# Performance work log

Measured on AMD Instinct MI355X. Metric: run time of the kernel, lower is better.

The kernel has to match this reference:

```python
import jax, jax.numpy as jnp
import numpy as np

DISCOUNT_FACTOR = 0.99
EPS = 1e-8


def setup_inputs() -> dict:
    key = jax.random.key(0)
    k1, k2, k3 = jax.random.split(key, 3)
    B, S = 8192, 1024
    # raw params initialized exactly like the torch module: atanh(target)
    raw_gamma = jnp.arctanh(jnp.array([DISCOUNT_FACTOR], dtype=jnp.float32))
    # create_init_lambda_sequence(0.5, S): linear ramp with mean == AVERAGE_LAMBDA
    lam_init = jnp.linspace(0.1, 0.9, S).astype(jnp.float32)
    raw_lambd = jnp.arctanh(lam_init)
    values = jax.random.normal(k1, (B, S + 1, 1), dtype=jnp.float32)
    rewards = jax.random.normal(k2, (B, S, 1), dtype=jnp.float32)
    dones = jax.random.randint(k3, (B, S, 1), 0, 2).astype(jnp.int32)
    return {
        "raw_gamma": raw_gamma,
        "raw_lambd": raw_lambd,
        "values": values,
        "rewards": rewards,
        "dones": dones,
        "input_seq_len": 1024,
    }


def reference(raw_gamma, raw_lambd, values, rewards, dones, input_seq_len):
    # gamma / lambd properties: tanh then clamp_min(1e-8)
    gamma = jnp.maximum(jnp.tanh(raw_gamma), EPS)[0]            # scalar
    lambd = jnp.maximum(jnp.tanh(raw_lambd), EPS)               # [max_seq_len]
    lam_seq = lambd[-input_seq_len:]                            # [S]

    # ---- update_sum_reward_weights (runs under no_grad in torch) ----
    # backward recurrence: v[t] = gamma * (1 - lam[t] + lam[t] * v[t+1]),  v[S] = 1
    def w_step(v_next, lam_t):
        v_t = gamma * (1.0 - lam_t + lam_t * v_next)
        return v_t, jnp.maximum(1.0 - v_t, EPS)

    _, w = jax.lax.scan(
        w_step,
        jnp.asarray(1.0, values.dtype),
        jax.lax.stop_gradient(lam_seq),
        reverse=True,
    )  # w: [S]
    srw = w / jnp.maximum(w.mean(), EPS)
    sum_reward_weights = jax.lax.stop_gradient(srw)[None, :, None]  # [1, S, 1]

    # ---- calculate_lambda_returns ----
    # ret[t] = r[t] + gamma*(1-done[t]) * ((1-lam[t])*V[t+1] + lam[t]*ret[t+1])
    d = dones.astype(values.dtype)
    v_next = values[:, 1:, :]                                   # [B, S, 1]
    xs = (
        jnp.swapaxes(rewards, 0, 1),   # [S, B, 1]
        jnp.swapaxes(d, 0, 1),         # [S, B, 1]
        jnp.swapaxes(v_next, 0, 1),    # [S, B, 1]
        lam_seq,                       # [S]
    )

    def r_step(ret_next, x):
        r, dn, vn, lam = x
        ret = r + gamma * (1.0 - dn) * ((1.0 - lam) * vn + lam * ret_next)
        return ret, ret

    _, rets = jax.lax.scan(r_step, values[:, -1, :], xs, reverse=True)  # [S, B, 1]
    lambda_returns = jnp.swapaxes(rets, 0, 1)                           # [B, S, 1]
    return lambda_returns, sum_reward_weights
```

## Files before the change

### kernel.cpp

```cpp
#include <hip/hip_runtime.h>
#include <math.h>

#define EPSF 1e-8f

typedef float fvec4 __attribute__((ext_vector_type(4), aligned(4)));

__device__ __forceinline__ void suffix_scan64(float& A, float& B, int lane) {
#pragma unroll
    for (int d = 1; d < 64; d <<= 1) {
        float Ao = __shfl_down(A, d);
        float Bo = __shfl_down(B, d);
        if (lane + d < 64) {
            A = fmaf(B, Ao, A);
            B = B * Bo;
        }
    }
}

__global__ __launch_bounds__(256)
void prep_kernel(const float* __restrict__ raw_gamma,
                 const float* __restrict__ raw_lambd, int lam_off,
                 float* __restrict__ gl, float* __restrict__ gol,
                 float* __restrict__ srw_out, int S)
{
    __shared__ float s_gl[1024];
    __shared__ float s_gol[1024];
    const float gamma = fmaxf(tanhf(raw_gamma[0]), EPSF);
    for (int t = threadIdx.x; t < S; t += 256) {
        float lam = fmaxf(tanhf(raw_lambd[lam_off + t]), EPSF);
        float g1 = gamma * lam;
        float g0 = gamma - g1;
        gl[t] = g1;  gol[t] = g0;
        s_gl[t] = g1; s_gol[t] = g0;
    }
    __syncthreads();
    if (threadIdx.x >= 64) return;
    const int lane = threadIdx.x;
    const int base = lane << 4;

    float a[16], b[16];
#pragma unroll
    for (int j = 0; j < 16; ++j) { a[j] = s_gol[base + j]; b[j] = s_gl[base + j]; }

    float A = a[15], Bc = b[15];
#pragma unroll
    for (int j = 14; j >= 0; --j) { A = fmaf(b[j], A, a[j]); Bc *= b[j]; }
    suffix_scan64(A, Bc, lane);
    float EA = __shfl_down(A, 1);
    float EB = __shfl_down(Bc, 1);
    if (lane == 63) { EA = 0.0f; EB = 1.0f; }

    float v = fmaf(EB, 1.0f, EA);
    float w[16];
    float sum = 0.0f;
#pragma unroll
    for (int j = 15; j >= 0; --j) {
        v = fmaf(b[j], v, a[j]);
        w[j] = fmaxf(1.0f - v, EPSF);
        sum += w[j];
    }
#pragma unroll
    for (int d = 32; d; d >>= 1) sum += __shfl_xor(sum, d);
    float inv = 1.0f / fmaxf(sum / (float)S, EPSF);
#pragma unroll
    for (int j = 0; j < 16; ++j) srw_out[base + j] = w[j] * inv;
}

__global__ __launch_bounds__(256, 4)
void td_main(const float* __restrict__ gl, const float* __restrict__ gol,
             const float* __restrict__ values,
             const float* __restrict__ rewards,
             const int* __restrict__ dones,
             float* __restrict__ out, int B, int S)
{
    const int lane = threadIdx.x & 63;
    const int b = blockIdx.x * 4 + (threadIdx.x >> 6);
    if (b >= B) return;

    const float* rrow = rewards + (size_t)b * S;
    const int*   drow = dones   + (size_t)b * S;
    const float* vrow = values  + (size_t)b * (S + 1);
    float*       orow = out     + (size_t)b * S;
    const int base = lane << 4;

    float4 r4[4]; int4 dd[4]; fvec4 v4[4]; float4 g1[4]; float4 g0[4];
#pragma unroll
    for (int k = 0; k < 4; ++k) {
        r4[k] = *(const float4*)(rrow + base + 4 * k);
        dd[k] = *(const int4*)(drow + base + 4 * k);
        v4[k] = *(const fvec4*)(vrow + base + 4 * k);
        g1[k] = *(const float4*)(gl + base + 4 * k);
        g0[k] = *(const float4*)(gol + base + 4 * k);
    }
    float vS = vrow[S];
    float vb = __shfl_down(v4[0].x, 1);
    if (lane == 63) vb = vS;

    float a[16], bb[16];
#pragma unroll
    for (int k = 0; k < 4; ++k) {
        float vn0 = v4[k].y, vn1 = v4[k].z, vn2 = v4[k].w;
        float vn3 = (k < 3) ? v4[k + 1].x : vb;
        float vn[4] = {vn0, vn1, vn2, vn3};
        float rr[4] = {r4[k].x, r4[k].y, r4[k].z, r4[k].w};
        int   di[4] = {dd[k].x, dd[k].y, dd[k].z, dd[k].w};
        float G1[4] = {g1[k].x, g1[k].y, g1[k].z, g1[k].w};
        float G0[4] = {g0[k].x, g0[k].y, g0[k].z, g0[k].w};
#pragma unroll
        for (int j = 0; j < 4; ++j) {
            float nd = 1.0f - (float)di[j];
            bb[4 * k + j] = G1[j] * nd;
            a[4 * k + j]  = fmaf(G0[j] * vn[j], nd, rr[j]);
        }
    }

    float A = a[15], Bc = bb[15];
#pragma unroll
    for (int j = 14; j >= 0; --j) { A = fmaf(bb[j], A, a[j]); Bc *= bb[j]; }

    suffix_scan64(A, Bc, lane);
    float EA = __shfl_down(A, 1);
    float EB = __shfl_down(Bc, 1);
    if (lane == 63) { EA = 0.0f; EB = 1.0f; }
    float x = fmaf(EB, vS, EA);

    float o[16];
#pragma unroll
    for (int j = 15; j >= 0; --j) {
        x = fmaf(bb[j], x, a[j]);
        o[j] = x;
    }
#pragma unroll
    for (int k = 0; k < 4; ++k)
        *(float4*)(orow + base + 4 * k) =
            make_float4(o[4 * k], o[4 * k + 1], o[4 * k + 2], o[4 * k + 3]);
}

extern "C" void kernel_launch(void* const* d_in, const int* in_sizes, int n_in,
                              void* d_out, int out_size, void* d_ws, size_t ws_size,
                              hipStream_t stream) {
    const float* raw_gamma = (const float*)d_in[0];
    const float* raw_lambd = (const float*)d_in[1];
    const float* values    = (const float*)d_in[2];
    const float* rewards   = (const float*)d_in[3];
    const int*   dones     = (const int*)d_in[4];
    float* out = (float*)d_out;

    int n_v = in_sizes[2];
    int n_r = in_sizes[3];
    int B = n_v - n_r;
    int S = n_r / B;
    int lam_off = in_sizes[1] - S;

    float* gl  = (float*)d_ws;
    float* gol = gl + S;
    float* srw_out = out + (size_t)B * S;

    prep_kernel<<<1, 256, 0, stream>>>(raw_gamma, raw_lambd, lam_off,
                                       gl, gol, srw_out, S);
    td_main<<<(B + 3) / 4, 256, 0, stream>>>(gl, gol, values, rewards, dones,
                                             out, B, S);
}
```

Baseline: 152.2 us.

## Fuse prep into main kernel and interleave per-lane chunks for coalescing

Merges the parameter-prep kernel into the main lambda-return kernel. Every block now recomputes gamma*lambda into shared memory, and one extra block writes the sum-reward weights, so one launch and the workspace round trip go away. Each lane now handles four strided chunks of 4 elements instead of 16 contiguous ones, which makes the float4 loads coalesced across the wave; a four-wide scan plus a serial combine of the chunk boundaries keeps the result exact. Outputs use nontemporal stores. The cost is redundant tanh work per block, more shuffles, and unaligned value loads at offset t+1.

```diff
diff --git a/kernel.cpp b/kernel.cpp
--- a/kernel.cpp
+++ b/kernel.cpp
@@ -4,6 +4,7 @@
 #define EPSF 1e-8f
 
 typedef float fvec4 __attribute__((ext_vector_type(4), aligned(4)));
+typedef float nvec4 __attribute__((ext_vector_type(4)));
 
 __device__ __forceinline__ void suffix_scan64(float& A, float& B, int lane) {
 #pragma unroll
@@ -17,11 +18,14 @@
     }
 }
 
-__global__ __launch_bounds__(256)
-void prep_kernel(const float* __restrict__ raw_gamma,
-                 const float* __restrict__ raw_lambd, int lam_off,
-                 float* __restrict__ gl, float* __restrict__ gol,
-                 float* __restrict__ srw_out, int S)
+__global__ __launch_bounds__(256, 4)
+void td_kernel(const float* __restrict__ raw_gamma,
+               const float* __restrict__ raw_lambd, int lam_off,
+               const float* __restrict__ values,
+               const float* __restrict__ rewards,
+               const int* __restrict__ dones,
+               float* __restrict__ out,
+               int B, int S, int rowBlocks)
 {
     __shared__ float s_gl[1024];
     __shared__ float s_gol[1024];
@@ -29,111 +33,138 @@
     for (int t = threadIdx.x; t < S; t += 256) {
         float lam = fmaxf(tanhf(raw_lambd[lam_off + t]), EPSF);
         float g1 = gamma * lam;
-        float g0 = gamma - g1;
-        gl[t] = g1;  gol[t] = g0;
-        s_gl[t] = g1; s_gol[t] = g0;
+        s_gl[t] = g1;
+        s_gol[t] = gamma - g1;
     }
     __syncthreads();
-    if (threadIdx.x >= 64) return;
-    const int lane = threadIdx.x;
-    const int base = lane << 4;
 
-    float a[16], b[16];
+    const int lane = threadIdx.x & 63;
+
+    if ((int)blockIdx.x == rowBlocks) {
+        if (threadIdx.x >= 64) return;
+        const int base = lane << 4;
+        float a[16], b[16];
 #pragma unroll
-    for (int j = 0; j < 16; ++j) { a[j] = s_gol[base + j]; b[j] = s_gl[base + j]; }
+        for (int j = 0; j < 16; ++j) { a[j] = s_gol[base + j]; b[j] = s_gl[base + j]; }
+        float A = a[15], Bc = b[15];
+#pragma unroll
+        for (int j = 14; j >= 0; --j) { A = fmaf(b[j], A, a[j]); Bc *= b[j]; }
+        suffix_scan64(A, Bc, lane);
+        float EA = __shfl_down(A, 1);
+        float EB = __shfl_down(Bc, 1);
+        if (lane == 63) { EA = 0.0f; EB = 1.0f; }
+        float v = EA + EB;
+        float w[16], sum = 0.0f;
+#pragma unroll
+        for (int j = 15; j >= 0; --j) {
+            v = fmaf(b[j], v, a[j]);
+            w[j] = fmaxf(1.0f - v, EPSF);
+            sum += w[j];
+        }
+#pragma unroll
+        for (int d = 32; d; d >>= 1) sum += __shfl_xor(sum, d);
+        float inv = 1.0f / fmaxf(sum / (float)S, EPSF);
+        float* srw = out + (size_t)B * S;
+#pragma unroll
+        for (int j = 0; j < 16; ++j) srw[base + j] = w[j] * inv;
+        return;
+    }
 
-    float A = a[15], Bc = b[15];
-#pragma unroll
-    for (int j = 14; j >= 0; --j) { A = fmaf(b[j], A, a[j]); Bc *= b[j]; }
-    suffix_scan64(A, Bc, lane);
-    float EA = __shfl_down(A, 1);
-    float EB = __shfl_down(Bc, 1);
-    if (lane == 63) { EA = 0.0f; EB = 1.0f; }
-
-    float v = fmaf(EB, 1.0f, EA);
-    float w[16];
-    float sum = 0.0f;
-#pragma unroll
-    for (int j = 15; j >= 0; --j) {
-        v = fmaf(b[j], v, a[j]);
-        w[j] = fmaxf(1.0f - v, EPSF);
-        sum += w[j];
-    }
-#pragma unroll
-    for (int d = 32; d; d >>= 1) sum += __shfl_xor(sum, d);
-    float inv = 1.0f / fmaxf(sum / (float)S, EPSF);
-#pragma unroll
-    for (int j = 0; j < 16; ++j) srw_out[base + j] = w[j] * inv;
-}
-
-__global__ __launch_bounds__(256, 4)
-void td_main(const float* __restrict__ gl, const float* __restrict__ gol,
-             const float* __restrict__ values,
-             const float* __restrict__ rewards,
-             const int* __restrict__ dones,
-             float* __restrict__ out, int B, int S)
-{
-    const int lane = threadIdx.x & 63;
     const int b = blockIdx.x * 4 + (threadIdx.x >> 6);
     if (b >= B) return;
+    const int C = S >> 2;
+    const int t0 = lane << 2;
 
     const float* rrow = rewards + (size_t)b * S;
     const int*   drow = dones   + (size_t)b * S;
     const float* vrow = values  + (size_t)b * (S + 1);
     float*       orow = out     + (size_t)b * S;
-    const int base = lane << 4;
 
-    float4 r4[4]; int4 dd[4]; fvec4 v4[4]; float4 g1[4]; float4 g0[4];
+    float4 r4[4]; int4 d4[4]; fvec4 v4[4];
 #pragma unroll
-    for (int k = 0; k < 4; ++k) {
-        r4[k] = *(const float4*)(rrow + base + 4 * k);
-        dd[k] = *(const int4*)(drow + base + 4 * k);
-        v4[k] = *(const fvec4*)(vrow + base + 4 * k);
-        g1[k] = *(const float4*)(gl + base + 4 * k);
-        g0[k] = *(const float4*)(gol + base + 4 * k);
+    for (int c = 0; c < 4; ++c) {
+        int t = c * C + t0;
+        r4[c] = *(const float4*)(rrow + t);
+        d4[c] = *(const int4*)(drow + t);
+        v4[c] = *(const fvec4*)(vrow + t + 1);
     }
     float vS = vrow[S];
-    float vb = __shfl_down(v4[0].x, 1);
-    if (lane == 63) vb = vS;
 
     float a[16], bb[16];
 #pragma unroll
-    for (int k = 0; k < 4; ++k) {
-        float vn0 = v4[k].y, vn1 = v4[k].z, vn2 = v4[k].w;
-        float vn3 = (k < 3) ? v4[k + 1].x : vb;
-        float vn[4] = {vn0, vn1, vn2, vn3};
-        float rr[4] = {r4[k].x, r4[k].y, r4[k].z, r4[k].w};
-        int   di[4] = {dd[k].x, dd[k].y, dd[k].z, dd[k].w};
-        float G1[4] = {g1[k].x, g1[k].y, g1[k].z, g1[k].w};
-        float G0[4] = {g0[k].x, g0[k].y, g0[k].z, g0[k].w};
+    for (int c = 0; c < 4; ++c) {
+        const float4 G1 = *(const float4*)&s_gl[c * C + t0];
+        const float4 G0 = *(const float4*)&s_gol[c * C + t0];
+        float vn[4] = {v4[c].x, v4[c].y, v4[c].z, v4[c].w};
+        float rr[4] = {r4[c].x, r4[c].y, r4[c].z, r4[c].w};
+        int   di[4] = {d4[c].x, d4[c].y, d4[c].z, d4[c].w};
+        float g1v[4] = {G1.x, G1.y, G1.z, G1.w};
+        float g0v[4] = {G0.x, G0.y, G0.z, G0.w};
 #pragma unroll
         for (int j = 0; j < 4; ++j) {
             float nd = 1.0f - (float)di[j];
-            bb[4 * k + j] = G1[j] * nd;
-            a[4 * k + j]  = fmaf(G0[j] * vn[j], nd, rr[j]);
+            bb[c * 4 + j] = g1v[j] * nd;
+            a[c * 4 + j]  = fmaf(g0v[j] * vn[j], nd, rr[j]);
         }
     }
 
-    float A = a[15], Bc = bb[15];
+    float A[4], Bc[4];
 #pragma unroll
-    for (int j = 14; j >= 0; --j) { A = fmaf(bb[j], A, a[j]); Bc *= bb[j]; }
+    for (int c = 0; c < 4; ++c) {
+        A[c] = a[c * 4 + 3]; Bc[c] = bb[c * 4 + 3];
+#pragma unroll
+        for (int j = 2; j >= 0; --j) {
+            A[c] = fmaf(bb[c * 4 + j], A[c], a[c * 4 + j]);
+            Bc[c] *= bb[c * 4 + j];
+        }
+    }
 
-    suffix_scan64(A, Bc, lane);
-    float EA = __shfl_down(A, 1);
-    float EB = __shfl_down(Bc, 1);
-    if (lane == 63) { EA = 0.0f; EB = 1.0f; }
-    float x = fmaf(EB, vS, EA);
+#pragma unroll
+    for (int d = 1; d < 64; d <<= 1) {
+        float Ao[4], Bo[4];
+#pragma unroll
+        for (int c = 0; c < 4; ++c) {
+            Ao[c] = __shfl_down(A[c], d);
+            Bo[c] = __shfl_down(Bc[c], d);
+        }
+        if (lane + d < 64) {
+#pragma unroll
+            for (int c = 0; c < 4; ++c) {
+                A[c] = fmaf(Bc[c], Ao[c], A[c]);
+                Bc[c] *= Bo[c];
+            }
+        }
+    }
 
-    float o[16];
+    float EA[4], EB[4], A0[4], B0[4];
 #pragma unroll
-    for (int j = 15; j >= 0; --j) {
-        x = fmaf(bb[j], x, a[j]);
-        o[j] = x;
+    for (int c = 0; c < 4; ++c) {
+        EA[c] = __shfl_down(A[c], 1);
+        EB[c] = __shfl_down(Bc[c], 1);
+        A0[c] = __shfl(A[c], 0);
+        B0[c] = __shfl(Bc[c], 0);
     }
+    if (lane == 63) {
 #pragma unroll
-    for (int k = 0; k < 4; ++k)
-        *(float4*)(orow + base + 4 * k) =
-            make_float4(o[4 * k], o[4 * k + 1], o[4 * k + 2], o[4 * k + 3]);
+        for (int c = 0; c < 4; ++c) { EA[c] = 0.0f; EB[c] = 1.0f; }
+    }
+
+    float x4 = vS;
+    float x3 = fmaf(B0[3], x4, A0[3]);
+    float x2 = fmaf(B0[2], x3, A0[2]);
+    float x1 = fmaf(B0[1], x2, A0[1]);
+    float xin[4] = {x1, x2, x3, x4};
+
+#pragma unroll
+    for (int c = 0; c < 4; ++c) {
+        float x  = fmaf(EB[c], xin[c], EA[c]);
+        float o3 = fmaf(bb[c * 4 + 3], x,  a[c * 4 + 3]);
+        float o2 = fmaf(bb[c * 4 + 2], o3, a[c * 4 + 2]);
+        float o1 = fmaf(bb[c * 4 + 1], o2, a[c * 4 + 1]);
+        float o0 = fmaf(bb[c * 4 + 0], o1, a[c * 4 + 0]);
+        nvec4 ov = {o0, o1, o2, o3};
+        __builtin_nontemporal_store(ov, (nvec4*)(orow + c * C + t0));
+    }
 }
 
 extern "C" void kernel_launch(void* const* d_in, const int* in_sizes, int n_in,
@@ -152,12 +183,8 @@
     int S = n_r / B;
     int lam_off = in_sizes[1] - S;
 
-    float* gl  = (float*)d_ws;
-    float* gol = gl + S;
-    float* srw_out = out + (size_t)B * S;
-
-    prep_kernel<<<1, 256, 0, stream>>>(raw_gamma, raw_lambd, lam_off,
-                                       gl, gol, srw_out, S);
-    td_main<<<(B + 3) / 4, 256, 0, stream>>>(gl, gol, values, rewards, dones,
-                                             out, B, S);
+    int rowBlocks = (B + 3) / 4;
+    td_kernel<<<rowBlocks + 1, 256, 0, stream>>>(
+        raw_gamma, raw_lambd, lam_off, values, rewards, dones,
+        out, B, S, rowBlocks);
 }
```

After: 146.8 us. 3.5% less time.

## Fuse prep into persistent row-loop kernel with register prefetch and block-wide scan

Applied to the files above, without the earlier changes.

Merges the lambda/weight prep kernel into the main kernel: every block recomputes gamma*lambda in shared memory, and one extra block writes the reward weights. The main work becomes a persistent loop where each block processes one row per iteration with 4 wavefronts splitting the sequence. Combining the wavefronts needs a shared-memory carry step and a __syncthreads per row. The next row's inputs are prefetched into registers and outputs use nontemporal stores. This removes one kernel launch and the workspace round trip and improves latency hiding, but every block now repeats 1024 tanh evaluations.

```diff
diff --git a/kernel.cpp b/kernel.cpp
--- a/kernel.cpp
+++ b/kernel.cpp
@@ -4,6 +4,7 @@
 #define EPSF 1e-8f
 
 typedef float fvec4 __attribute__((ext_vector_type(4), aligned(4)));
+typedef float nvec4 __attribute__((ext_vector_type(4)));
 
 __device__ __forceinline__ void suffix_scan64(float& A, float& B, int lane) {
 #pragma unroll
@@ -17,123 +18,118 @@
     }
 }
 
-__global__ __launch_bounds__(256)
-void prep_kernel(const float* __restrict__ raw_gamma,
-                 const float* __restrict__ raw_lambd, int lam_off,
-                 float* __restrict__ gl, float* __restrict__ gol,
-                 float* __restrict__ srw_out, int S)
+__global__ __launch_bounds__(256, 8)
+void td_kernel(const float* __restrict__ raw_gamma,
+               const float* __restrict__ raw_lambd, int lam_off,
+               const float* __restrict__ values,
+               const float* __restrict__ rewards,
+               const int* __restrict__ dones,
+               float* __restrict__ out,
+               int B, int S, int rowBlocks)
 {
     __shared__ float s_gl[1024];
-    __shared__ float s_gol[1024];
+    __shared__ float sA[2][4], sB[2][4];
     const float gamma = fmaxf(tanhf(raw_gamma[0]), EPSF);
-    for (int t = threadIdx.x; t < S; t += 256) {
-        float lam = fmaxf(tanhf(raw_lambd[lam_off + t]), EPSF);
-        float g1 = gamma * lam;
-        float g0 = gamma - g1;
-        gl[t] = g1;  gol[t] = g0;
-        s_gl[t] = g1; s_gol[t] = g0;
+    for (int t = threadIdx.x; t < S; t += 256)
+        s_gl[t] = gamma * fmaxf(tanhf(raw_lambd[lam_off + t]), EPSF);
+    __syncthreads();
+
+    const int lane = threadIdx.x & 63;
+    const int c    = threadIdx.x >> 6;
+
+    if ((int)blockIdx.x == rowBlocks) {
+        if (threadIdx.x >= 64) return;
+        const int base = lane << 4;
+        float a[16], b[16];
+#pragma unroll
+        for (int j = 0; j < 16; ++j) { b[j] = s_gl[base + j]; a[j] = gamma - b[j]; }
+        float A = a[15], Bc = b[15];
+#pragma unroll
+        for (int j = 14; j >= 0; --j) { A = fmaf(b[j], A, a[j]); Bc *= b[j]; }
+        suffix_scan64(A, Bc, lane);
+        float EA = __shfl_down(A, 1);
+        float EB = __shfl_down(Bc, 1);
+        if (lane == 63) { EA = 0.0f; EB = 1.0f; }
+        float v = EA + EB;
+        float w[16], sum = 0.0f;
+#pragma unroll
+        for (int j = 15; j >= 0; --j) {
+            v = fmaf(b[j], v, a[j]);
+            w[j] = fmaxf(1.0f - v, EPSF);
+            sum += w[j];
+        }
+#pragma unroll
+        for (int d = 32; d; d >>= 1) sum += __shfl_xor(sum, d);
+        float inv = 1.0f / fmaxf(sum / (float)S, EPSF);
+        float* srw = out + (size_t)B * S;
+#pragma unroll
+        for (int j = 0; j < 16; ++j) srw[base + j] = w[j] * inv;
+        return;
     }
-    __syncthreads();
-    if (threadIdx.x >= 64) return;
-    const int lane = threadIdx.x;
-    const int base = lane << 4;
 
-    float a[16], b[16];
-#pragma unroll
-    for (int j = 0; j < 16; ++j) { a[j] = s_gol[base + j]; b[j] = s_gl[base + j]; }
+    const int t0 = (c << 8) + (lane << 2);
+    const float4 G1 = *(const float4*)&s_gl[t0];
+    const float g1v[4] = {G1.x, G1.y, G1.z, G1.w};
+    const float g0v[4] = {gamma - G1.x, gamma - G1.y, gamma - G1.z, gamma - G1.w};
 
-    float A = a[15], Bc = b[15];
-#pragma unroll
-    for (int j = 14; j >= 0; --j) { A = fmaf(b[j], A, a[j]); Bc *= b[j]; }
-    suffix_scan64(A, Bc, lane);
-    float EA = __shfl_down(A, 1);
-    float EB = __shfl_down(Bc, 1);
-    if (lane == 63) { EA = 0.0f; EB = 1.0f; }
+    float4 cr; int4 cd; fvec4 cv; float cvS;
+    {
+        const int r = blockIdx.x;
+        cr  = *(const float4*)(rewards + (size_t)r * S + t0);
+        cd  = *(const int4*)(dones + (size_t)r * S + t0);
+        cv  = *(const fvec4*)(values + (size_t)r * (S + 1) + t0 + 1);
+        cvS = values[(size_t)r * (S + 1) + S];
+    }
 
-    float v = fmaf(EB, 1.0f, EA);
-    float w[16];
-    float sum = 0.0f;
-#pragma unroll
-    for (int j = 15; j >= 0; --j) {
-        v = fmaf(b[j], v, a[j]);
-        w[j] = fmaxf(1.0f - v, EPSF);
-        sum += w[j];
-    }
-#pragma unroll
-    for (int d = 32; d; d >>= 1) sum += __shfl_xor(sum, d);
-    float inv = 1.0f / fmaxf(sum / (float)S, EPSF);
-#pragma unroll
-    for (int j = 0; j < 16; ++j) srw_out[base + j] = w[j] * inv;
-}
+    int p = 0;
+#pragma unroll 1
+    for (int r = blockIdx.x; r < B; r += rowBlocks) {
+        const int rn = r + rowBlocks;
+        float4 nr; int4 nd; fvec4 nv; float nvS = 0.0f;
+        if (rn < B) {
+            nr  = *(const float4*)(rewards + (size_t)rn * S + t0);
+            nd  = *(const int4*)(dones + (size_t)rn * S + t0);
+            nv  = *(const fvec4*)(values + (size_t)rn * (S + 1) + t0 + 1);
+            nvS = values[(size_t)rn * (S + 1) + S];
+        }
 
-__global__ __launch_bounds__(256, 4)
-void td_main(const float* __restrict__ gl, const float* __restrict__ gol,
-             const float* __restrict__ values,
-             const float* __restrict__ rewards,
-             const int* __restrict__ dones,
-             float* __restrict__ out, int B, int S)
-{
-    const int lane = threadIdx.x & 63;
-    const int b = blockIdx.x * 4 + (threadIdx.x >> 6);
-    if (b >= B) return;
-
-    const float* rrow = rewards + (size_t)b * S;
-    const int*   drow = dones   + (size_t)b * S;
-    const float* vrow = values  + (size_t)b * (S + 1);
-    float*       orow = out     + (size_t)b * S;
-    const int base = lane << 4;
-
-    float4 r4[4]; int4 dd[4]; fvec4 v4[4]; float4 g1[4]; float4 g0[4];
-#pragma unroll
-    for (int k = 0; k < 4; ++k) {
-        r4[k] = *(const float4*)(rrow + base + 4 * k);
-        dd[k] = *(const int4*)(drow + base + 4 * k);
-        v4[k] = *(const fvec4*)(vrow + base + 4 * k);
-        g1[k] = *(const float4*)(gl + base + 4 * k);
-        g0[k] = *(const float4*)(gol + base + 4 * k);
-    }
-    float vS = vrow[S];
-    float vb = __shfl_down(v4[0].x, 1);
-    if (lane == 63) vb = vS;
-
-    float a[16], bb[16];
-#pragma unroll
-    for (int k = 0; k < 4; ++k) {
-        float vn0 = v4[k].y, vn1 = v4[k].z, vn2 = v4[k].w;
-        float vn3 = (k < 3) ? v4[k + 1].x : vb;
-        float vn[4] = {vn0, vn1, vn2, vn3};
-        float rr[4] = {r4[k].x, r4[k].y, r4[k].z, r4[k].w};
-        int   di[4] = {dd[k].x, dd[k].y, dd[k].z, dd[k].w};
-        float G1[4] = {g1[k].x, g1[k].y, g1[k].z, g1[k].w};
-        float G0[4] = {g0[k].x, g0[k].y, g0[k].z, g0[k].w};
+        float vn[4] = {cv.x, cv.y, cv.z, cv.w};
+        float rr[4] = {cr.x, cr.y, cr.z, cr.w};
+        int   di[4] = {cd.x, cd.y, cd.z, cd.w};
+        float a[4], b[4];
 #pragma unroll
         for (int j = 0; j < 4; ++j) {
-            float nd = 1.0f - (float)di[j];
-            bb[4 * k + j] = G1[j] * nd;
-            a[4 * k + j]  = fmaf(G0[j] * vn[j], nd, rr[j]);
+            float ndn = 1.0f - (float)di[j];
+            b[j] = g1v[j] * ndn;
+            a[j] = fmaf(g0v[j] * vn[j], ndn, rr[j]);
         }
+
+        float A = a[3], Bc = b[3];
+#pragma unroll
+        for (int j = 2; j >= 0; --j) { A = fmaf(b[j], A, a[j]); Bc *= b[j]; }
+        suffix_scan64(A, Bc, lane);
+        float EA = __shfl_down(A, 1);
+        float EB = __shfl_down(Bc, 1);
+        if (lane == 63) { EA = 0.0f; EB = 1.0f; }
+        if (lane == 0) { sA[p][c] = A; sB[p][c] = Bc; }
+        __syncthreads();
+
+        float x = cvS;
+#pragma unroll
+        for (int j = 3; j >= 1; --j)
+            if (j > c) x = fmaf(sB[p][j], x, sA[p][j]);
+
+        float xi = fmaf(EB, x, EA);
+        float o3 = fmaf(b[3], xi, a[3]);
+        float o2 = fmaf(b[2], o3, a[2]);
+        float o1 = fmaf(b[1], o2, a[1]);
+        float o0 = fmaf(b[0], o1, a[0]);
+        nvec4 ov = {o0, o1, o2, o3};
+        __builtin_nontemporal_store(ov, (nvec4*)(out + (size_t)r * S + t0));
+
+        if (rn < B) { cr = nr; cd = nd; cv = nv; cvS = nvS; }
+        p ^= 1;
     }
-
-    float A = a[15], Bc = bb[15];
-#pragma unroll
-    for (int j = 14; j >= 0; --j) { A = fmaf(bb[j], A, a[j]); Bc *= bb[j]; }
-
-    suffix_scan64(A, Bc, lane);
-    float EA = __shfl_down(A, 1);
-    float EB = __shfl_down(Bc, 1);
-    if (lane == 63) { EA = 0.0f; EB = 1.0f; }
-    float x = fmaf(EB, vS, EA);
-
-    float o[16];
-#pragma unroll
-    for (int j = 15; j >= 0; --j) {
-        x = fmaf(bb[j], x, a[j]);
-        o[j] = x;
-    }
-#pragma unroll
-    for (int k = 0; k < 4; ++k)
-        *(float4*)(orow + base + 4 * k) =
-            make_float4(o[4 * k], o[4 * k + 1], o[4 * k + 2], o[4 * k + 3]);
 }
 
 extern "C" void kernel_launch(void* const* d_in, const int* in_sizes, int n_in,
@@ -152,12 +148,9 @@
     int S = n_r / B;
     int lam_off = in_sizes[1] - S;
 
-    float* gl  = (float*)d_ws;
-    float* gol = gl + S;
-    float* srw_out = out + (size_t)B * S;
-
-    prep_kernel<<<1, 256, 0, stream>>>(raw_gamma, raw_lambd, lam_off,
-                                       gl, gol, srw_out, S);
-    td_main<<<(B + 3) / 4, 256, 0, stream>>>(gl, gol, values, rewards, dones,
-                                             out, B, S);
+    int rowBlocks = 2048;
+    if (rowBlocks > B) rowBlocks = B;
+    td_kernel<<<rowBlocks + 1, 256, 0, stream>>>(
+        raw_gamma, raw_lambd, lam_off, values, rewards, dones,
+        out, B, S, rowBlocks);
 }
```

Result: faster. 142.7 us (-6.2%).
